# Performance work log

Hardware: AMD Instinct MI355X
Metric: run time of the kernel (lower is better)

Reference implementation:

```python
import jax, jax.numpy as jnp
import numpy as np

NNZ = 16777216  # 2**24 nonzeros
D = 2048        # dense size (D, D, D); sum over dim 2 -> (D, D)


def setup_inputs() -> dict:
    key = jax.random.key(0)
    kv, ki = jax.random.split(key)
    values = jax.random.normal(kv, (NNZ,), dtype=jnp.float32)
    indices = jax.random.randint(ki, (3, NNZ), 0, D, dtype=jnp.int64)
    return {"values": values, "indices": indices}


def reference(values, indices):
    # sparse_coo_tensor(indices, values, size=(D,D,D)) -> sparse.sum(dim=2) -> to_dense()
    # is equivalent to a scatter-add of values keyed by (indices[0], indices[1]):
    # the third index only distinguishes entries that get summed away, and COO
    # coalescing already sums duplicate coordinates.
    out = jnp.zeros((D, D), dtype=jnp.float32)
    out = out.at[indices[0], indices[1]].add(values)
    return out
```

## Files before the change

kernel.cpp:

```cpp
#include <hip/hip_runtime.h>

#define NNZ 16777216
#define D 2048
#define NB 256
#define ROWS_PER_B 8
#define T1 512
#define EPT 16
#define CHUNK 8192
#define NCHUNK (NNZ / CHUNK)
#define SEG 8960
#define T2 512
#define NW (T2 / 64)
#define RUNS (NCHUNK / NW)
#define DEPTH 8

__global__ __launch_bounds__(T1) void bin_scatter(
    const float* __restrict__ values,
    const int* __restrict__ idx0,
    const int* __restrict__ idx1,
    unsigned int* __restrict__ dump,
    unsigned int* __restrict__ pptab)
{
    __shared__ unsigned int lhist[NB];
    __shared__ unsigned int ppref[NB];
    __shared__ unsigned int wsum[4];
    __shared__ unsigned int stage[SEG];

    const int tid = threadIdx.x;
    if (tid < NB) lhist[tid] = 0;
    __syncthreads();

    const int vecBase = blockIdx.x * (CHUNK / 4);

    float4 v[4]; int4 a[4]; int4 c[4];
#pragma unroll
    for (int it = 0; it < 4; ++it) {
        int g = vecBase + it * T1 + tid;
        v[it] = reinterpret_cast<const float4*>(values)[g];
        a[it] = reinterpret_cast<const int4*>(idx0)[g];
        c[it] = reinterpret_cast<const int4*>(idx1)[g];
    }

    unsigned int outw[EPT];
    unsigned int meta[EPT];
#pragma unroll
    for (int it = 0; it < 4; ++it) {
        const int*   ap = reinterpret_cast<const int*>(&a[it]);
        const int*   cp = reinterpret_cast<const int*>(&c[it]);
        const float* vp = reinterpret_cast<const float*>(&v[it]);
#pragma unroll
        for (int e = 0; e < 4; ++e) {
            int i0 = ap[e], i1 = cp[e];
            unsigned int b = (unsigned int)i0 >> 3;
            unsigned int fb = __float_as_uint(vp[e]);
            unsigned int bf = (fb + 0x7fffu + ((fb >> 16) & 1u)) >> 16;
            outw[it * 4 + e] = ((((unsigned int)(i0 & 7) << 11) | (unsigned int)i1) << 16) | bf;
            unsigned int rk = atomicAdd(&lhist[b], 1u);
            meta[it * 4 + e] = (b << 16) | rk;
        }
    }
    __syncthreads();

    unsigned int x = 0, pc = 0, cnt = 0;
    if (tid < NB) {
        const int lane = tid & 63;
        cnt = lhist[tid];
        pc = (cnt + 3u) & ~3u;
        x = pc;
#pragma unroll
        for (int dlt = 1; dlt < 64; dlt <<= 1) {
            unsigned int y = __shfl_up(x, dlt, 64);
            if (lane >= dlt) x += y;
        }
        if (lane == 63) wsum[tid >> 6] = x;
    }
    __syncthreads();
    if (tid < NB) {
        const int wid = tid >> 6;
        unsigned int off = 0;
#pragma unroll
        for (int w = 0; w < 4; ++w) off += (w < wid) ? wsum[w] : 0u;
        unsigned int excl = x - pc + off;
        ppref[tid] = excl;
        pptab[(size_t)blockIdx.x * NB + tid] = (excl << 16) | cnt;
    }
    __syncthreads();

#pragma unroll
    for (int e = 0; e < EPT; ++e) {
        unsigned int b  = meta[e] >> 16;
        unsigned int rk = meta[e] & 0xFFFFu;
        stage[ppref[b] + rk] = outw[e];
    }
    __syncthreads();

    const uint4* s4 = reinterpret_cast<const uint4*>(stage);
    uint4* d4 = reinterpret_cast<uint4*>(dump + (size_t)blockIdx.x * SEG);
    for (int j = tid; j < SEG / 4; j += T1)
        d4[j] = s4[j];
}

__global__ __launch_bounds__(T2) void bucket_accumulate(
    const unsigned int* __restrict__ dump,
    const unsigned int* __restrict__ pptab,
    float* __restrict__ out)
{
    __shared__ float tile[ROWS_PER_B * D];

    const int b = blockIdx.x;
    const int tid = threadIdx.x;
    const int w = tid >> 6;
    const int lane = tid & 63;

    for (int j = tid; j < ROWS_PER_B * D / 4; j += T2)
        reinterpret_cast<float4*>(tile)[j] = make_float4(0.f, 0.f, 0.f, 0.f);
    __syncthreads();

    unsigned int pc0, pc1, pc2, pc3, pc4, pc5, pc6, pc7;
    unsigned int wd0, wd1, wd2, wd3, wd4, wd5, wd6, wd7;

#define PFX(jj) pptab[(size_t)(w + NW * (jj)) * NB + b]
#define PAYLOAD(jj, pcv)  \
    ((lane < (int)((pcv) & 0xFFFFu)) \
        ? dump[(size_t)(w + NW * (jj)) * SEG + ((pcv) >> 16) + lane] : 0u)

    pc0 = PFX(0); pc1 = PFX(1); pc2 = PFX(2); pc3 = PFX(3);
    pc4 = PFX(4); pc5 = PFX(5); pc6 = PFX(6); pc7 = PFX(7);
    wd0 = PAYLOAD(0, pc0); wd1 = PAYLOAD(1, pc1);
    wd2 = PAYLOAD(2, pc2); wd3 = PAYLOAD(3, pc3);
    wd4 = PAYLOAD(4, pc4); wd5 = PAYLOAD(5, pc5);
    wd6 = PAYLOAD(6, pc6); wd7 = PAYLOAD(7, pc7);

#define PSTEP(i, pcv, wdv) { \
    if (wdv) atomicAdd(&tile[wdv >> 16], __uint_as_float(wdv << 16)); \
    unsigned int c_ = pcv & 0xFFFFu; \
    if (c_ > 64u) {                        \
        const unsigned int* base_ = dump + (size_t)(w + NW * (j + i)) * SEG + (pcv >> 16); \
        for (unsigned int t_ = 64u + lane; t_ < c_; t_ += 64u) { \
            unsigned int ww_ = base_[t_]; \
            if (ww_) atomicAdd(&tile[ww_ >> 16], __uint_as_float(ww_ << 16)); \
        } \
    } \
    int jn_ = j + i + DEPTH; \
    if (jn_ < RUNS) { \
        unsigned int pcn_ = PFX(jn_); \
        wdv = PAYLOAD(jn_, pcn_); \
        pcv = pcn_; \
    } else { wdv = 0u; pcv = 0u; } \
}

    for (int j = 0; j < RUNS; j += DEPTH) {
        PSTEP(0, pc0, wd0) PSTEP(1, pc1, wd1) PSTEP(2, pc2, wd2) PSTEP(3, pc3, wd3)
        PSTEP(4, pc4, wd4) PSTEP(5, pc5, wd5) PSTEP(6, pc6, wd6) PSTEP(7, pc7, wd7)
    }
#undef PSTEP
#undef PAYLOAD
#undef PFX
    __syncthreads();

    float4* o4 = reinterpret_cast<float4*>(out + (size_t)b * ROWS_PER_B * D);
    for (int j = tid; j < ROWS_PER_B * D / 4; j += T2)
        o4[j] = reinterpret_cast<float4*>(tile)[j];
}

__global__ __launch_bounds__(256) void scatter_add_kernel(
    const float* __restrict__ values,
    const int* __restrict__ idx0,
    const int* __restrict__ idx1,
    float* __restrict__ out)
{
    const int nvec = NNZ / 4;
    int tid = blockIdx.x * blockDim.x + threadIdx.x;
    int stride = gridDim.x * blockDim.x;
    for (int i = tid; i < nvec; i += stride) {
        const float4 v = reinterpret_cast<const float4*>(values)[i];
        const int4   a = reinterpret_cast<const int4*>(idx0)[i];
        const int4   b = reinterpret_cast<const int4*>(idx1)[i];
        atomicAdd(&out[a.x * D + b.x], v.x);
        atomicAdd(&out[a.y * D + b.y], v.y);
        atomicAdd(&out[a.z * D + b.z], v.z);
        atomicAdd(&out[a.w * D + b.w], v.w);
    }
}

extern "C" void kernel_launch(void* const* d_in, const int* in_sizes, int n_in,
                              void* d_out, int out_size, void* d_ws, size_t ws_size,
                              hipStream_t stream) {
    const float* values  = (const float*)d_in[0];
    const int*   indices = (const int*)d_in[1];
    const int*   idx0 = indices;
    const int*   idx1 = indices + NNZ;
    float* out = (float*)d_out;

    const size_t pp_bytes = (size_t)NCHUNK * NB * sizeof(unsigned int);
    const size_t need = pp_bytes + (size_t)NCHUNK * SEG * sizeof(unsigned int);

    if (ws_size < need) {
        hipMemsetAsync(out, 0, (size_t)out_size * sizeof(float), stream);
        const int nvec = NNZ / 4;
        scatter_add_kernel<<<(nvec + 255) / 256, 256, 0, stream>>>(values, idx0, idx1, out);
        return;
    }

    unsigned int* pptab = (unsigned int*)d_ws;
    unsigned int* dump  = (unsigned int*)((char*)d_ws + pp_bytes);

    bin_scatter<<<NCHUNK, T1, 0, stream>>>(values, idx0, idx1, dump, pptab);
    bucket_accumulate<<<NB, T2, 0, stream>>>(dump, pptab, out);
}
```

Measured before the change: 157.2 us.

## Transpose per-chunk bucket descriptor table and stage it in LDS

The chunk-by-bucket descriptor table is now written transposed, so each accumulate block reads its bucket's descriptors as one contiguous coalesced run and caches them in shared memory. Each wave also now handles a contiguous range of chunks instead of interleaved ones. This removes strided, latency-bound global loads of descriptors from the accumulate loop. In exchange, the producer kernel's descriptor writes become strided, and the accumulate kernel uses 8 KB more LDS per block.

```diff
diff --git a/kernel.cpp b/kernel.cpp
--- a/kernel.cpp
+++ b/kernel.cpp
@@ -19,7 +19,7 @@
     const int* __restrict__ idx0,
     const int* __restrict__ idx1,
     unsigned int* __restrict__ dump,
-    unsigned int* __restrict__ pptab)
+    unsigned int* __restrict__ pptabT)
 {
     __shared__ unsigned int lhist[NB];
     __shared__ unsigned int ppref[NB];
@@ -82,7 +82,7 @@
         for (int w = 0; w < 4; ++w) off += (w < wid) ? wsum[w] : 0u;
         unsigned int excl = x - pc + off;
         ppref[tid] = excl;
-        pptab[(size_t)blockIdx.x * NB + tid] = (excl << 16) | cnt;
+        pptabT[(size_t)tid * NCHUNK + blockIdx.x] = (excl << 16) | cnt;
     }
     __syncthreads();
 
@@ -102,10 +102,11 @@
 
 __global__ __launch_bounds__(T2) void bucket_accumulate(
     const unsigned int* __restrict__ dump,
-    const unsigned int* __restrict__ pptab,
+    const unsigned int* __restrict__ pptabT,
     float* __restrict__ out)
 {
     __shared__ float tile[ROWS_PER_B * D];
+    __shared__ unsigned int sdesc[NCHUNK];
 
     const int b = blockIdx.x;
     const int tid = threadIdx.x;
@@ -114,37 +115,40 @@
 
     for (int j = tid; j < ROWS_PER_B * D / 4; j += T2)
         reinterpret_cast<float4*>(tile)[j] = make_float4(0.f, 0.f, 0.f, 0.f);
-    __syncthreads();
+    for (int j = tid; j < NCHUNK; j += T2)
+        sdesc[j] = pptabT[(size_t)b * NCHUNK + j];
+    __syncthreads();
+
+    const unsigned int k0 = (unsigned int)w * RUNS;
 
     unsigned int pc0, pc1, pc2, pc3, pc4, pc5, pc6, pc7;
     unsigned int wd0, wd1, wd2, wd3, wd4, wd5, wd6, wd7;
 
-#define PFX(jj) pptab[(size_t)(w + NW * (jj)) * NB + b]
-#define PAYLOAD(jj, pcv)  \
+#define PAYLOAD(kn, pcv) \
     ((lane < (int)((pcv) & 0xFFFFu)) \
-        ? dump[(size_t)(w + NW * (jj)) * SEG + ((pcv) >> 16) + lane] : 0u)
-
-    pc0 = PFX(0); pc1 = PFX(1); pc2 = PFX(2); pc3 = PFX(3);
-    pc4 = PFX(4); pc5 = PFX(5); pc6 = PFX(6); pc7 = PFX(7);
-    wd0 = PAYLOAD(0, pc0); wd1 = PAYLOAD(1, pc1);
-    wd2 = PAYLOAD(2, pc2); wd3 = PAYLOAD(3, pc3);
-    wd4 = PAYLOAD(4, pc4); wd5 = PAYLOAD(5, pc5);
-    wd6 = PAYLOAD(6, pc6); wd7 = PAYLOAD(7, pc7);
+        ? dump[(kn) * SEG + ((pcv) >> 16) + (unsigned)lane] : 0u)
+
+    pc0 = sdesc[k0 + 0]; pc1 = sdesc[k0 + 1]; pc2 = sdesc[k0 + 2]; pc3 = sdesc[k0 + 3];
+    pc4 = sdesc[k0 + 4]; pc5 = sdesc[k0 + 5]; pc6 = sdesc[k0 + 6]; pc7 = sdesc[k0 + 7];
+    wd0 = PAYLOAD(k0 + 0, pc0); wd1 = PAYLOAD(k0 + 1, pc1);
+    wd2 = PAYLOAD(k0 + 2, pc2); wd3 = PAYLOAD(k0 + 3, pc3);
+    wd4 = PAYLOAD(k0 + 4, pc4); wd5 = PAYLOAD(k0 + 5, pc5);
+    wd6 = PAYLOAD(k0 + 6, pc6); wd7 = PAYLOAD(k0 + 7, pc7);
 
 #define PSTEP(i, pcv, wdv) { \
     if (wdv) atomicAdd(&tile[wdv >> 16], __uint_as_float(wdv << 16)); \
     unsigned int c_ = pcv & 0xFFFFu; \
     if (c_ > 64u) {                        \
-        const unsigned int* base_ = dump + (size_t)(w + NW * (j + i)) * SEG + (pcv >> 16); \
-        for (unsigned int t_ = 64u + lane; t_ < c_; t_ += 64u) { \
+        const unsigned int* base_ = dump + (k0 + (unsigned)(j + i)) * SEG + (pcv >> 16); \
+        for (unsigned int t_ = 64u + (unsigned)lane; t_ < c_; t_ += 64u) { \
             unsigned int ww_ = base_[t_]; \
             if (ww_) atomicAdd(&tile[ww_ >> 16], __uint_as_float(ww_ << 16)); \
         } \
     } \
     int jn_ = j + i + DEPTH; \
     if (jn_ < RUNS) { \
-        unsigned int pcn_ = PFX(jn_); \
-        wdv = PAYLOAD(jn_, pcn_); \
+        unsigned int pcn_ = sdesc[k0 + (unsigned)jn_];    \
+        wdv = PAYLOAD(k0 + (unsigned)jn_, pcn_); \
         pcv = pcn_; \
     } else { wdv = 0u; pcv = 0u; } \
 }
@@ -155,7 +159,6 @@
     }
 #undef PSTEP
 #undef PAYLOAD
-#undef PFX
     __syncthreads();
 
     float4* o4 = reinterpret_cast<float4*>(out + (size_t)b * ROWS_PER_B * D);
@@ -192,7 +195,7 @@
     const int*   idx1 = indices + NNZ;
     float* out = (float*)d_out;
 
-    const size_t pp_bytes = (size_t)NCHUNK * NB * sizeof(unsigned int);
+    const size_t pp_bytes = (size_t)NB * NCHUNK * sizeof(unsigned int);
     const size_t need = pp_bytes + (size_t)NCHUNK * SEG * sizeof(unsigned int);
 
     if (ws_size < need) {
@@ -202,9 +205,9 @@
         return;
     }
 
-    unsigned int* pptab = (unsigned int*)d_ws;
-    unsigned int* dump  = (unsigned int*)((char*)d_ws + pp_bytes);
-
-    bin_scatter<<<NCHUNK, T1, 0, stream>>>(values, idx0, idx1, dump, pptab);
-    bucket_accumulate<<<NB, T2, 0, stream>>>(dump, pptab, out);
-}
+    unsigned int* pptabT = (unsigned int*)d_ws;
+    unsigned int* dump   = (unsigned int*)((char*)d_ws + pp_bytes);
+
+    bin_scatter<<<NCHUNK, T1, 0, stream>>>(values, idx0, idx1, dump, pptabT);
+    bucket_accumulate<<<NB, T2, 0, stream>>>(dump, pptabT, out);
+}
```

Measured after the change: 150.8 us. 1.04x faster.
